# Performance work log

Measured on AMD Instinct MI355X. Metric: run time of the kernel, lower is better.

The kernel has to match this reference:

```python
import jax, jax.numpy as jnp
import numpy as np

M, B, S, D, H = 3, 32, 256, 768, 1024
LN_EPS = 1e-5


def _ln(x, g, b):
    m = jnp.mean(x, axis=-1, keepdims=True)
    v = jnp.mean((x - m) ** 2, axis=-1, keepdims=True)
    return (x - m) / jnp.sqrt(v + LN_EPS) * g + b


def setup_inputs() -> dict:
    key = jax.random.key(0)
    ks = jax.random.split(key, 16)
    sc = 0.02  # weight init scale
    return {
        "feats": jax.random.normal(ks[0], (M, B, S, D), jnp.float32),
        "Wq": jax.random.normal(ks[1], (M, D, D), jnp.float32) * sc,
        "bq": jnp.zeros((M, D), jnp.float32),
        "Wk": jax.random.normal(ks[2], (M, D, D), jnp.float32) * sc,
        "bk": jnp.zeros((M, D), jnp.float32),
        "Wv": jax.random.normal(ks[3], (M, D, D), jnp.float32) * sc,
        "bv": jnp.zeros((M, D), jnp.float32),
        "pgq_w": jax.random.normal(ks[4], (M, D), jnp.float32) * sc,
        "pgq_b": jnp.zeros((M,), jnp.float32),
        "pgk_w": jax.random.normal(ks[5], (M, D), jnp.float32) * sc,
        "pgk_b": jnp.zeros((M,), jnp.float32),
        "mu_w": jax.random.normal(ks[6], (M, D), jnp.float32) * sc,
        "mu_b": jnp.zeros((M,), jnp.float32),
        "lv_w": jax.random.normal(ks[7], (M, D), jnp.float32) * sc,
        "lv_b": jnp.zeros((M,), jnp.float32),
        "dyn": jnp.ones((1,), jnp.float32),
        "WE_w": jax.random.normal(ks[8], (M, D, D), jnp.float32) * sc,
        "WE_b": jnp.zeros((M, D), jnp.float32),
        "Wh_w": jax.random.normal(ks[9], (M, D, D), jnp.float32) * sc,
        "Wh_b": jnp.zeros((M, D), jnp.float32),
        "Wqc_w": jax.random.normal(ks[10], (M, D, D), jnp.float32) * sc,
        "Wqc_b": jnp.zeros((M, D), jnp.float32),
        "lnE_g": jnp.ones((M, D), jnp.float32),
        "lnE_b": jnp.zeros((M, D), jnp.float32),
        "lnG_g": jnp.ones((M, D), jnp.float32),
        "lnG_b": jnp.zeros((M, D), jnp.float32),
        "out_w": jax.random.normal(ks[11], (D * M, H), jnp.float32) * sc,
        "out_b": jnp.zeros((H,), jnp.float32),
        "eps": jax.random.normal(ks[12], (M, M - 1, B, S, 1), jnp.float32),
    }


def reference(feats, Wq, bq, Wk, bk, Wv, bv, pgq_w, pgq_b, pgk_w, pgk_b,
              mu_w, mu_b, lv_w, lv_b, dyn, WE_w, WE_b, Wh_w, Wh_b, Wqc_w, Wqc_b,
              lnE_g, lnE_b, lnG_g, lnG_b, out_w, out_b, eps):
    # batched per-modality projections: [M,B,S,D]
    Qs = jnp.einsum('mbsd,mde->mbse', feats, Wq) + bq[:, None, None, :]
    Ks = jnp.einsum('mbsd,mde->mbse', feats, Wk) + bk[:, None, None, :]
    Vs = jnp.einsum('mbsd,mde->mbse', feats, Wv) + bv[:, None, None, :]
    scale = 1.0 / jnp.sqrt(jnp.float32(D))

    kl = jnp.float32(0.0)
    outs = []
    for i in range(M):
        Qi = Qs[i]  # [B,S,D]
        mu = jnp.einsum('bsd,d->bs', Qi, mu_w[i])[..., None] + mu_b[i]      # [B,S,1]
        lv = jnp.einsum('bsd,d->bs', Qi, lv_w[i])[..., None] + lv_b[i]      # [B,S,1]
        std = jnp.exp(0.5 * lv)
        pq_base = jax.nn.sigmoid(
            jnp.einsum('bsd,d->bs', Qi, pgq_w[i])[..., None] + pgq_b[i])    # [B,S,1]
        kl_i = -0.5 * jnp.sum(1.0 + lv - mu ** 2 - jnp.exp(lv))
        agg = jnp.zeros_like(Qi)
        cnt = 0
        for j in range(M):
            if j == i:
                continue
            d_gate = mu + dyn * std * eps[i, cnt]  # reparameterization
            cnt += 1
            kl = kl + kl_i
            g = jax.nn.sigmoid(d_gate)             # [B,S,1]
            p_q = pq_base * g
            p_k = jax.nn.sigmoid(
                jnp.einsum('bsd,d->bs', Ks[j], pgk_w[i])[..., None] + pgk_b[i]) * g
            A = jnp.einsum('bqd,bkd->bqk', Qi, Ks[j]) * scale
            A = A * p_q * jnp.swapaxes(p_k, 1, 2)  # pregated scores
            W = jax.nn.softmax(A, axis=-1)
            agg = agg + jnp.einsum('bqk,bkd->bqd', W, Vs[j])
        # CAG
        E = jax.nn.relu(agg @ WE_w[i] + WE_b[i])
        G = jax.nn.relu(agg @ Wh_w[i] + Wh_b[i] + Qi @ Wqc_w[i] + Wqc_b[i])
        Ci = _ln(E, lnE_g[i], lnE_b[i]) * _ln(G, lnG_g[i], lnG_b[i])
        outs.append(Ci)
    fused = jnp.concatenate(outs, axis=-1)[:, 0, :]  # [B, M*D]
    out = fused @ out_w + out_b                       # [B, H]
    return out, kl
```

## Files before the change

### kernel.cpp

```cpp
#include <hip/hip_runtime.h>

#define M 3
#define B 32
#define S 256
#define D 768
#define H 1024
#define MD (M * D)
#define NP (M * (M - 1))
#define SCALE 0.03608439182435161f
#define LN_EPS 1e-5f

#define OFF_WMU   0
#define OFF_WLV   2304
#define OFF_WPGQ  4608
#define OFF_WPK   6912
#define OFF_CMU   11520
#define OFF_CLV   11523
#define OFF_CPGQ  11526
#define OFF_CPK   11529
#define OFF_PQ    11536
#define OFF_Q     11776
#define OFF_QBK   85504
#define OFF_QK    85760
#define OFF_MLH   233216
#define OFF_KLP   236288
#define OFF_FUSED 457728
#define OFF_FSUM  531520
#define OFF_WKT   1711168
#define OFF_ARENA 3480640
#define OFF_ARENA2 7019584
#define OFF_AGG   236544

__device__ __forceinline__ float wave_reduce(float v) {
    #pragma unroll
    for (int o = 32; o > 0; o >>= 1) v += __shfl_down(v, o, 64);
    return v;
}

__device__ __forceinline__ float sigmoidf(float x) {
    return 1.0f / (1.0f + __expf(-x));
}

__device__ __forceinline__ float dot4(float4 a, float4 b) {
    return a.x * b.x + a.y * b.y + a.z * b.z + a.w * b.w;
}

__device__ __forceinline__ void fma4(float4& a, float s, float4 w) {
    a.x += s * w.x; a.y += s * w.y; a.z += s * w.z; a.w += s * w.w;
}

__global__ __launch_bounds__(256) void k_prep2(const float* feats,
        const float* Wq, const float* Wk,
        const float* bq, const float* bk,
        const float* mu_w, const float* mu_b, const float* lv_w, const float* lv_b,
        const float* pgq_w, const float* pgq_b, const float* pgk_w, const float* pgk_b,
        float* ws) {
    int blk = blockIdx.x;
    if (blk < 72) {
        int mat = blk / 12, rg = blk % 12;
        const float* Wm; const float *va, *vb, *vc;
        float *oa, *ob, *oc; int nv;
        if (mat < 3) {
            int i = mat;
            Wm = Wq + i * D * D;
            va = mu_w + i * D; vb = lv_w + i * D; vc = pgq_w + i * D;
            oa = ws + OFF_WMU + i * D; ob = ws + OFF_WLV + i * D; oc = ws + OFF_WPGQ + i * D;
            nv = 3;
        } else {
            int j = mat - 3;
            int i1 = (j == 0) ? 1 : 0, i2 = (j == 2) ? 1 : 2;
            int p1 = 2 * i1 + ((j < i1) ? j : j - 1);
            int p2 = 2 * i2 + ((j < i2) ? j : j - 1);
            Wm = Wk + j * D * D;
            va = pgk_w + i1 * D; vb = pgk_w + i2 * D; vc = va;
            oa = ws + OFF_WPK + p1 * D; ob = ws + OFF_WPK + p2 * D; oc = oa;
            nv = 2;
        }
        int wave = threadIdx.x >> 6, lane = threadIdx.x & 63;
        const float4* va4 = (const float4*)va;
        const float4* vb4 = (const float4*)vb;
        const float4* vc4 = (const float4*)vc;
        float4 A0 = va4[lane], A1 = va4[lane + 64], A2 = va4[lane + 128];
        float4 B0 = vb4[lane], B1 = vb4[lane + 64], B2 = vb4[lane + 128];
        float4 C0 = vc4[lane], C1 = vc4[lane + 64], C2 = vc4[lane + 128];
        int base = rg * 64 + wave * 16;
        for (int r = 0; r < 16; r += 2) {
            const float4* rowP = (const float4*)(Wm + (base + r) * D);
            const float4* rowQ = (const float4*)(Wm + (base + r + 1) * D);
            float4 x0 = rowP[lane], x1 = rowP[lane + 64], x2 = rowP[lane + 128];
            float4 y0 = rowQ[lane], y1 = rowQ[lane + 64], y2 = rowQ[lane + 128];
            float daP = dot4(x0, A0) + dot4(x1, A1) + dot4(x2, A2);
            float dbP = dot4(x0, B0) + dot4(x1, B1) + dot4(x2, B2);
            float dcP = dot4(x0, C0) + dot4(x1, C1) + dot4(x2, C2);
            float daQ = dot4(y0, A0) + dot4(y1, A1) + dot4(y2, A2);
            float dbQ = dot4(y0, B0) + dot4(y1, B1) + dot4(y2, B2);
            float dcQ = dot4(y0, C0) + dot4(y1, C1) + dot4(y2, C2);
            daP = wave_reduce(daP); dbP = wave_reduce(dbP);
            daQ = wave_reduce(daQ); dbQ = wave_reduce(dbQ);
            if (nv == 3) { dcP = wave_reduce(dcP); dcQ = wave_reduce(dcQ); }
            if (lane == 0) {
                oa[base + r] = daP; ob[base + r] = dbP;
                oa[base + r + 1] = daQ; ob[base + r + 1] = dbQ;
                if (nv == 3) { oc[base + r] = dcP; oc[base + r + 1] = dcQ; }
            }
        }
    } else if (blk < 87) {
        int job = blk - 72;
        const float *a, *bvec; float bias; float* out;
        if (job < 3)      { int i = job;     a = bq + i * D; bvec = mu_w + i * D;  bias = mu_b[i];  out = ws + OFF_CMU + i; }
        else if (job < 6) { int i = job - 3; a = bq + i * D; bvec = lv_w + i * D;  bias = lv_b[i];  out = ws + OFF_CLV + i; }
        else if (job < 9) { int i = job - 6; a = bq + i * D; bvec = pgq_w + i * D; bias = pgq_b[i]; out = ws + OFF_CPGQ + i; }
        else {
            int p = job - 9, i = p / 2, c = p % 2, j = c + (c >= i ? 1 : 0);
            a = bk + j * D; bvec = pgk_w + i * D; bias = pgk_b[i]; out = ws + OFF_CPK + p;
        }
        int t = threadIdx.x;
        float part = 0.f;
        if (t < 192) part = dot4(((const float4*)a)[t], ((const float4*)bvec)[t]);
        part = wave_reduce(part);
        __shared__ float r[4];
        if ((t & 63) == 0) r[t >> 6] = part;
        __syncthreads();
        if (t == 0) *out = r[0] + r[1] + r[2] + r[3] + bias;
    } else if (blk < 519) {
        int r = blk - 87;
        int j = r / 144; r = r % 144;
        int d0 = (r / 12) * 64, e0 = (r % 12) * 64;
        __shared__ float tile[64][65];
        const float* src = Wk + j * D * D;
        for (int idx = threadIdx.x; idx < 4096; idx += 256) {
            int rr = idx / 64, cc = idx % 64;
            tile[rr][cc] = src[(d0 + rr) * D + e0 + cc];
        }
        __syncthreads();
        float* dst = ws + OFF_WKT + j * D * D;
        for (int idx = threadIdx.x; idx < 4096; idx += 256) {
            int rr = idx / 64, cc = idx % 64;
            dst[(e0 + rr) * D + d0 + cc] = tile[cc][rr];
        }
    } else {
        int qb = blk - 519;
        int i = qb / 96, r = qb % 96, bg = r / 24, kc = r % 24;
        int kbase = kc * 32;
        __shared__ __align__(16) float xs[32][8];
        for (int idx = threadIdx.x; idx < 256; idx += 256) {
            int d = idx & 31, bb = idx >> 5;
            xs[d][bb] = feats[((size_t)(i * B + bg * 8 + bb) * S) * D + kbase + d];
        }
        __syncthreads();
        if (threadIdx.x < 192) {
            int e4 = threadIdx.x * 4;
            const float* Wm = Wq + i * D * D + kbase * D + e4;
            float4 acc[8];
            #pragma unroll
            for (int bb = 0; bb < 8; bb++) acc[bb] = make_float4(0.f, 0.f, 0.f, 0.f);
            for (int k = 0; k < 32; k++) {
                float4 w = *(const float4*)(Wm + k * D);
                float4 x0 = *(const float4*)&xs[k][0];
                float4 x1 = *(const float4*)&xs[k][4];
                fma4(acc[0], x0.x, w); fma4(acc[1], x0.y, w);
                fma4(acc[2], x0.z, w); fma4(acc[3], x0.w, w);
                fma4(acc[4], x1.x, w); fma4(acc[5], x1.y, w);
                fma4(acc[6], x1.z, w); fma4(acc[7], x1.w, w);
            }
            #pragma unroll
            for (int bb = 0; bb < 8; bb++)
                *(float4*)&ws[OFF_ARENA + kc * 73728 + (i * 32 + bg * 8 + bb) * 768 + e4] = acc[bb];
        }
    }
}

__global__ __launch_bounds__(256) void k_redQ(const float* feats, const float* bq,
        const float* bk, const float* eps, const float* dyn, float* ws) {
    int blk = blockIdx.x;
    int i = blk / B, b = blk % B;
    int fbase = (i * B + b) * D;
    int t = threadIdx.x;
    int wave = t >> 6, lane = t & 63;
    __shared__ float4 qsh[192];
    __shared__ float redsh[8];
    __shared__ float pqred[12];
    if (t < 192) {
        float4 a = *(const float4*)&bq[i * D + t * 4];
        #pragma unroll
        for (int kc = 0; kc < 24; kc++) {
            float4 v = *(const float4*)&ws[OFF_ARENA + kc * 73728 + fbase + t * 4];
            a.x += v.x; a.y += v.y; a.z += v.z; a.w += v.w;
        }
        *(float4*)&ws[OFF_Q + fbase + t * 4] = a;
        qsh[t] = a;
    }
    __syncthreads();
    int jA = (i == 0) ? 1 : 0, jB = (i == 2) ? 1 : 2;
    float pA_ = 0.f, pB_ = 0.f;
    if (t < 192) {
        float4 q = qsh[t];
        pA_ = dot4(q, *(const float4*)&bk[jA * D + t * 4]);
        pB_ = dot4(q, *(const float4*)&bk[jB * D + t * 4]);
    }
    pA_ = wave_reduce(pA_); pB_ = wave_reduce(pB_);
    if (lane == 0) { redsh[wave] = pA_; redsh[4 + wave] = pB_; }
    float dm = 0.f, dl = 0.f, dp = 0.f;
    if (t < 192) {
        float4 x = *(const float4*)&feats[((size_t)(i * B + b) * S) * D + t * 4];
        dm = dot4(x, *(const float4*)&ws[OFF_WMU + i * D + t * 4]);
        dl = dot4(x, *(const float4*)&ws[OFF_WLV + i * D + t * 4]);
        dp = dot4(x, *(const float4*)&ws[OFF_WPGQ + i * D + t * 4]);
    }
    dm = wave_reduce(dm); dl = wave_reduce(dl); dp = wave_reduce(dp);
    if (lane == 0 && wave < 3) { pqred[wave] = dm; pqred[4 + wave] = dl; pqred[8 + wave] = dp; }
    __syncthreads();
    if (t == 0) {
        ws[OFF_QBK + (2 * i) * B + b]     = redsh[0] + redsh[1] + redsh[2] + redsh[3];
        ws[OFF_QBK + (2 * i + 1) * B + b] = redsh[4] + redsh[5] + redsh[6] + redsh[7];
        float mu0 = pqred[0] + pqred[1] + pqred[2] + ws[OFF_CMU + i];
        float lv0 = pqred[4] + pqred[5] + pqred[6] + ws[OFF_CLV + i];
        float pqb = pqred[8] + pqred[9] + pqred[10] + ws[OFF_CPGQ + i];
        float sd = dyn[0] * __expf(0.5f * lv0);
        float pqs = sigmoidf(pqb);
        #pragma unroll
        for (int c = 0; c < 2; c++) {
            int p = 2 * i + c;
            float e0 = eps[(size_t)(p * B + b) * S];
            ws[OFF_PQ + p * B + b] = pqs * sigmoidf(mu0 + sd * e0);
        }
    }
}

__global__ __launch_bounds__(256, 4) void k_qk(float* ws) {
    int blk = blockIdx.x;
    int j = blk / 192, r = blk % 192, vg = r / 24, kc = r % 24;
    int kbase = kc * 32;
    int i1 = (j == 0) ? 1 : 0, i2 = (j == 2) ? 1 : 2;
    __shared__ __align__(16) float xs[32][8];
    for (int idx = threadIdx.x; idx < 256; idx += 256) {
        int d = idx & 31, v = idx >> 5;
        int v64 = vg * 8 + v;
        int i_ = (v64 < 32) ? i1 : i2, b = v64 & 31;
        xs[d][v] = ws[OFF_Q + (i_ * 32 + b) * 768 + kbase + d];
    }
    __syncthreads();
    if (threadIdx.x < 192) {
        int e4 = threadIdx.x * 4;
        const float* Wm = ws + OFF_WKT + j * D * D + kbase * D + e4;
        float4 acc[8];
        #pragma unroll
        for (int bb = 0; bb < 8; bb++) acc[bb] = make_float4(0.f, 0.f, 0.f, 0.f);
        for (int k = 0; k < 32; k++) {
            float4 w = *(const float4*)(Wm + k * D);
            float4 x0 = *(const float4*)&xs[k][0];
            float4 x1 = *(const float4*)&xs[k][4];
            fma4(acc[0], x0.x, w); fma4(acc[1], x0.y, w);
            fma4(acc[2], x0.z, w); fma4(acc[3], x0.w, w);
            fma4(acc[4], x1.x, w); fma4(acc[5], x1.y, w);
            fma4(acc[6], x1.z, w); fma4(acc[7], x1.w, w);
        }
        #pragma unroll
        for (int v = 0; v < 8; v++)
            *(float4*)&ws[OFF_ARENA2 + kc * 147456 + (j * 64 + vg * 8 + v) * 768 + e4] = acc[v];
    }
}

__global__ __launch_bounds__(256) void k_redqk(float* ws) {
    int idx = blockIdx.x * 256 + threadIdx.x;
    int fidx = idx * 4;
    int row = fidx / 768, d = fidx % 768;
    int j = row / 64, v64 = row % 64;
    int b = v64 & 31, islot = v64 >> 5;
    int i_ = islot ? ((j == 2) ? 1 : 2) : ((j == 0) ? 1 : 0);
    int p = 2 * i_ + ((j < i_) ? j : j - 1);
    float4 a = make_float4(0.f, 0.f, 0.f, 0.f);
    #pragma unroll
    for (int kc = 0; kc < 24; kc++) {
        float4 v = *(const float4*)&ws[OFF_ARENA2 + kc * 147456 + fidx];
        a.x += v.x; a.y += v.y; a.z += v.z; a.w += v.w;
    }
    *(float4*)&ws[OFF_QK + (p * B + b) * D + d] = a;
}

__global__ __launch_bounds__(1024) void k_fused(const float* feats, const float* eps,
                                                const float* dyn, float* ws) {
    int blk = blockIdx.x;
    int b = blk >> 3, h = blk & 7;
    int t = threadIdx.x;
    int w = t >> 6, lane = t & 63;
    __shared__ __align__(16) float swA[4608];
    __shared__ __align__(16) float swPK[4608];
    __shared__ __align__(16) float sqk[4608];
    __shared__ float raws[6][32], pkps[6][32], mus[3][32], lvs[3][32], wgt[6][32];
    __shared__ float klv[96];
    __shared__ float pq_s[6], qbk_s[6], cmu_s[3], clv_s[3], cpk_s[6];
    {
        const float4* srcA = (const float4*)(ws + OFF_WMU);
        const float4* srcP = (const float4*)(ws + OFF_WPK);
        float4* dA = (float4*)swA;
        float4* dP = (float4*)swPK;
        float4* dQ = (float4*)sqk;
        for (int idx = t; idx < 1152; idx += 1024) {
            dA[idx] = srcA[idx];
            dP[idx] = srcP[idx];
            int p = idx / 192, d4 = (idx % 192) * 4;
            dQ[idx] = *(const float4*)&ws[OFF_QK + (p * B + b) * D + d4];
        }
        if (t < 6) { pq_s[t] = ws[OFF_PQ + t * B + b]; qbk_s[t] = ws[OFF_QBK + t * B + b]; cpk_s[t] = ws[OFF_CPK + t]; }
        else if (t < 9) { cmu_s[t - 6] = ws[OFF_CMU + t - 6]; clv_s[t - 6] = ws[OFF_CLV + t - 6]; }
    }
    __syncthreads();
    const float4* swA4 = (const float4*)swA;
    const float4* swPK4 = (const float4*)swPK;
    const float4* sqk4 = (const float4*)sqk;
    for (int tau = w * 6; tau < w * 6 + 6; tau++) {
        int m = tau >> 5, k = tau & 31;
        const float4* row = (const float4*)(feats + ((size_t)((m * B + b) * S) + h * 32 + k) * D);
        float4 x0 = row[lane], x1 = row[lane + 64], x2 = row[lane + 128];
        int i1 = (m == 0) ? 1 : 0, i2 = (m == 2) ? 1 : 2;
        int pj0 = 2 * i1 + ((m < i1) ? m : m - 1);
        int pj1 = 2 * i2 + ((m < i2) ? m : m - 1);
        int oM = m * 192, oL = (3 + m) * 192, o0 = pj0 * 192, o1 = pj1 * 192;
        float dmu = dot4(x0, swA4[oM + lane]) + dot4(x1, swA4[oM + lane + 64]) + dot4(x2, swA4[oM + lane + 128]);
        float dlv = dot4(x0, swA4[oL + lane]) + dot4(x1, swA4[oL + lane + 64]) + dot4(x2, swA4[oL + lane + 128]);
        float dk0 = dot4(x0, swPK4[o0 + lane]) + dot4(x1, swPK4[o0 + lane + 64]) + dot4(x2, swPK4[o0 + lane + 128]);
        float dk1 = dot4(x0, swPK4[o1 + lane]) + dot4(x1, swPK4[o1 + lane + 64]) + dot4(x2, swPK4[o1 + lane + 128]);
        float dr0 = dot4(x0, sqk4[o0 + lane]) + dot4(x1, sqk4[o0 + lane + 64]) + dot4(x2, sqk4[o0 + lane + 128]);
        float dr1 = dot4(x0, sqk4[o1 + lane]) + dot4(x1, sqk4[o1 + lane + 64]) + dot4(x2, sqk4[o1 + lane + 128]);
        dmu = wave_reduce(dmu); dlv = wave_reduce(dlv);
        dk0 = wave_reduce(dk0); dk1 = wave_reduce(dk1);
        dr0 = wave_reduce(dr0); dr1 = wave_reduce(dr1);
        if (lane == 0) {
            mus[m][k] = dmu + cmu_s[m];
            lvs[m][k] = dlv + clv_s[m];
            pkps[pj0][k] = dk0 + cpk_s[pj0];
            pkps[pj1][k] = dk1 + cpk_s[pj1];
            raws[pj0][k] = dr0;
            raws[pj1][k] = dr1;
        }
    }
    __syncthreads();
    float dynv = dyn[0];
    if (t < 192) {
        int p = t >> 5, k = t & 31;
        int iq = p >> 1;
        float e = eps[(size_t)(p * B + b) * S + h * 32 + k];
        float g = sigmoidf(mus[iq][k] + dynv * __expf(0.5f * lvs[iq][k]) * e);
        float pk = sigmoidf(pkps[p][k]) * g;
        float s = (raws[p][k] + qbk_s[p]) * SCALE * pq_s[p] * pk;
        float mc = s;
        #pragma unroll
        for (int o = 16; o > 0; o >>= 1) mc = fmaxf(mc, __shfl_xor(mc, o, 64));
        float wv_ = __expf(s - mc);
        float l = wv_;
        #pragma unroll
        for (int o = 16; o > 0; o >>= 1) l += __shfl_xor(l, o, 64);
        wgt[p][k] = wv_;
        if (k == 0) {
            float* mh = ws + OFF_MLH + (p * B + b) * 16 + h * 2;
            mh[0] = mc; mh[1] = l;
        }
    } else if (t < 288) {
        int tau = t - 192;
        int m = tau >> 5, k = tau & 31;
        float muv = mus[m][k], lvv = lvs[m][k];
        klv[tau] = 1.0f + lvv - muv * muv - __expf(lvv);
    }
    __syncthreads();
    if (t < 768) {
        #pragma unroll
        for (int jm = 0; jm < 3; jm++) {
            int i1 = (jm == 0) ? 1 : 0, i2 = (jm == 2) ? 1 : 2;
            int pj0 = 2 * i1 + ((jm < i1) ? jm : jm - 1);
            int pj1 = 2 * i2 + ((jm < i2) ? jm : jm - 1);
            const float* col = feats + ((size_t)((jm * B + b) * S) + h * 32) * D + t;
            float accA = 0.f, accB = 0.f;
            #pragma unroll 8
            for (int k = 0; k < 32; k++) {
                float fv = col[(size_t)k * D];
                accA += wgt[pj0][k] * fv;
                accB += wgt[pj1][k] * fv;
            }
            ws[OFF_FSUM + h * 147456 + (pj0 * B + b) * D + t] = accA;
            ws[OFF_FSUM + h * 147456 + (pj1 * B + b) * D + t] = accB;
        }
    }
    if (t < 64) {
        float s2 = klv[t] + ((t < 32) ? klv[64 + t] : 0.f);
        s2 = wave_reduce(s2);
        if (t == 0) ws[OFF_KLP + blk] = s2;
    }
}

__global__ __launch_bounds__(192, 4) void k_agg2(const float* Wv, float* ws) {
    int blk = blockIdx.x;
    int i = blk / 192, r = blk % 192, js = r / 96, r2 = r % 96, bg = r2 / 24, kc = r2 % 24;
    int kbase = kc * 32;
    int j0 = (i == 0) ? 1 : 0, j1 = (i == 2) ? 1 : 2;
    int jv = js ? j1 : j0;
    int p = 2 * i + js;
    __shared__ __align__(16) float xs[32][8];
    __shared__ float comb[8][8];
    if (threadIdx.x < 8) {
        int bb = threadIdx.x;
        const float* mh = ws + OFF_MLH + (p * B + bg * 8 + bb) * 16;
        float mm[8], ll[8];
        float mx = -1e30f;
        #pragma unroll
        for (int hh = 0; hh < 8; hh++) { mm[hh] = mh[2 * hh]; ll[hh] = mh[2 * hh + 1]; mx = fmaxf(mx, mm[hh]); }
        float L = 0.f;
        float ee[8];
        #pragma unroll
        for (int hh = 0; hh < 8; hh++) { ee[hh] = __expf(mm[hh] - mx); L += ee[hh] * ll[hh]; }
        #pragma unroll
        for (int hh = 0; hh < 8; hh++) comb[hh][bb] = ee[hh] / L;
    }
    __syncthreads();
    for (int idx = threadIdx.x; idx < 256; idx += 192) {
        int d = idx & 31, bb = idx >> 5;
        int base = OFF_FSUM + (p * B + bg * 8 + bb) * D + kbase + d;
        float v = 0.f;
        #pragma unroll
        for (int hh = 0; hh < 8; hh++) v += comb[hh][bb] * ws[base + hh * 147456];
        xs[d][bb] = v;
    }
    __syncthreads();
    int e4 = threadIdx.x * 4;
    const float* W0 = Wv + jv * D * D + kbase * D + e4;
    float4 acc[8];
    #pragma unroll
    for (int bb = 0; bb < 8; bb++) acc[bb] = make_float4(0.f, 0.f, 0.f, 0.f);
    for (int k = 0; k < 32; k++) {
        float4 w0 = *(const float4*)(W0 + k * D);
        float4 a0 = *(const float4*)&xs[k][0];
        float4 a1 = *(const float4*)&xs[k][4];
        fma4(acc[0], a0.x, w0); fma4(acc[1], a0.y, w0);
        fma4(acc[2], a0.z, w0); fma4(acc[3], a0.w, w0);
        fma4(acc[4], a1.x, w0); fma4(acc[5], a1.y, w0);
        fma4(acc[6], a1.z, w0); fma4(acc[7], a1.w, w0);
    }
    #pragma unroll
    for (int bb = 0; bb < 8; bb++)
        *(float4*)&ws[OFF_ARENA + (js * 24 + kc) * 73728 + (i * 32 + bg * 8 + bb) * 768 + e4] = acc[bb];
}

__global__ __launch_bounds__(256) void k_redA(const float* bv, float* ws) {
    int idx = blockIdx.x * 256 + threadIdx.x;
    int fidx = idx * 4;
    int i = fidx / 24576, e = fidx % 768;
    int j0 = (i == 0) ? 1 : 0, j1 = (i == 2) ? 1 : 2;
    float4 b0 = *(const float4*)&bv[j0 * 768 + e];
    float4 b1 = *(const float4*)&bv[j1 * 768 + e];
    float4 a = make_float4(b0.x + b1.x, b0.y + b1.y, b0.z + b1.z, b0.w + b1.w);
    #pragma unroll
    for (int s = 0; s < 48; s++) {
        float4 p = *(const float4*)&ws[OFF_ARENA + s * 73728 + fidx];
        a.x += p.x; a.y += p.y; a.z += p.z; a.w += p.w;
    }
    *(float4*)&ws[OFF_AGG + fidx] = a;
}

__global__ __launch_bounds__(192, 4) void k_eg2(const float* WE_w, const float* Wh_w,
                                                const float* Wqc_w, float* ws) {
    int blk = blockIdx.x;
    int kind = blk / 288, r = blk % 288;
    int i = r / 96, r2 = r % 96, bg = r2 / 24, kc = r2 % 24;
    int kbase = kc * 32;
    int src = (kind == 2) ? OFF_Q : OFF_AGG;
    __shared__ __align__(16) float xs[32][8];
    for (int idx = threadIdx.x; idx < 256; idx += 192) {
        int d = idx & 31, bb = idx >> 5;
        xs[d][bb] = ws[src + (i * 32 + bg * 8 + bb) * 768 + kbase + d];
    }
    __syncthreads();
    int e4 = threadIdx.x * 4;
    const float* Wm = ((kind == 0) ? WE_w : (kind == 1) ? Wh_w : Wqc_w) + i * D * D + kbase * D + e4;
    float4 acc[8];
    #pragma unroll
    for (int bb = 0; bb < 8; bb++) acc[bb] = make_float4(0.f, 0.f, 0.f, 0.f);
    for (int k = 0; k < 32; k++) {
        float4 w = *(const float4*)(Wm + k * D);
        float4 a0 = *(const float4*)&xs[k][0];
        float4 a1 = *(const float4*)&xs[k][4];
        fma4(acc[0], a0.x, w); fma4(acc[1], a0.y, w);
        fma4(acc[2], a0.z, w); fma4(acc[3], a0.w, w);
        fma4(acc[4], a1.x, w); fma4(acc[5], a1.y, w);
        fma4(acc[6], a1.z, w); fma4(acc[7], a1.w, w);
    }
    #pragma unroll
    for (int bb = 0; bb < 8; bb++)
        *(float4*)&ws[OFF_ARENA2 + (kind * 24 + kc) * 73728 + (i * 32 + bg * 8 + bb) * 768 + e4] = acc[bb];
}

__global__ __launch_bounds__(256) void k_redEGLN(const float* WE_b, const float* Wh_b,
        const float* Wqc_b,
        const float* lnE_g, const float* lnE_b,
        const float* lnG_g, const float* lnG_b, float* ws) {
    int blk = blockIdx.x;
    int i = blk / B, b = blk % B;
    int row = (i * B + b) * D;
    int t = threadIdx.x;
    float4 e = make_float4(0.f, 0.f, 0.f, 0.f);
    float4 g = make_float4(0.f, 0.f, 0.f, 0.f);
    if (t < 192) {
        e = *(const float4*)&WE_b[i * D + t * 4];
        float4 b0 = *(const float4*)&Wh_b[i * D + t * 4];
        float4 b1 = *(const float4*)&Wqc_b[i * D + t * 4];
        g = make_float4(b0.x + b1.x, b0.y + b1.y, b0.z + b1.z, b0.w + b1.w);
        #pragma unroll
        for (int s = 0; s < 24; s++) {
            float4 p = *(const float4*)&ws[OFF_ARENA2 + s * 73728 + row + t * 4];
            e.x += p.x; e.y += p.y; e.z += p.z; e.w += p.w;
        }
        #pragma unroll
        for (int s = 24; s < 72; s++) {
            float4 p = *(const float4*)&ws[OFF_ARENA2 + s * 73728 + row + t * 4];
            g.x += p.x; g.y += p.y; g.z += p.z; g.w += p.w;
        }
        e.x = fmaxf(e.x, 0.f); e.y = fmaxf(e.y, 0.f); e.z = fmaxf(e.z, 0.f); e.w = fmaxf(e.w, 0.f);
        g.x = fmaxf(g.x, 0.f); g.y = fmaxf(g.y, 0.f); g.z = fmaxf(g.z, 0.f); g.w = fmaxf(g.w, 0.f);
    }
    __shared__ float r1[256], r2[256], r3[256], r4[256];
    r1[t] = e.x + e.y + e.z + e.w;
    r2[t] = e.x * e.x + e.y * e.y + e.z * e.z + e.w * e.w;
    r3[t] = g.x + g.y + g.z + g.w;
    r4[t] = g.x * g.x + g.y * g.y + g.z * g.z + g.w * g.w;
    __syncthreads();
    for (int st = 128; st > 0; st >>= 1) {
        if (t < st) { r1[t] += r1[t + st]; r2[t] += r2[t + st]; r3[t] += r3[t + st]; r4[t] += r4[t + st]; }
        __syncthreads();
    }
    float mE = r1[0] * (1.0f / D), vE = r2[0] * (1.0f / D) - mE * mE;
    float mG = r3[0] * (1.0f / D), vG = r4[0] * (1.0f / D) - mG * mG;
    float sE = rsqrtf(vE + LN_EPS), sG = rsqrtf(vG + LN_EPS);
    if (t < 192) {
        float4 eg  = *(const float4*)&lnE_g[i * D + t * 4];
        float4 ebv = *(const float4*)&lnE_b[i * D + t * 4];
        float4 gg  = *(const float4*)&lnG_g[i * D + t * 4];
        float4 gbv = *(const float4*)&lnG_b[i * D + t * 4];
        float4 o;
        o.x = ((e.x - mE) * sE * eg.x + ebv.x) * ((g.x - mG) * sG * gg.x + gbv.x);
        o.y = ((e.y - mE) * sE * eg.y + ebv.y) * ((g.y - mG) * sG * gg.y + gbv.y);
        o.z = ((e.z - mE) * sE * eg.z + ebv.z) * ((g.z - mG) * sG * gg.z + gbv.z);
        o.w = ((e.w - mE) * sE * eg.w + ebv.w) * ((g.w - mG) * sG * gg.w + gbv.w);
        *(float4*)&ws[OFF_FUSED + b * MD + i * D + t * 4] = o;
    }
}

__global__ __launch_bounds__(256, 4) void k_out2(const float* out_w, float* ws) {
    int blk = blockIdx.x;
    int bg = blk / 72, kc = blk % 72;
    int kbase = kc * 32;
    __shared__ __align__(16) float xs[32][8];
    for (int idx = threadIdx.x; idx < 256; idx += 256) {
        int d = idx & 31, bb = idx >> 5;
        xs[d][bb] = ws[OFF_FUSED + (bg * 8 + bb) * MD + kbase + d];
    }
    __syncthreads();
    int e4 = threadIdx.x * 4;
    const float* Wm = out_w + kbase * H + e4;
    float4 acc[8];
    #pragma unroll
    for (int bb = 0; bb < 8; bb++) acc[bb] = make_float4(0.f, 0.f, 0.f, 0.f);
    for (int k = 0; k < 32; k++) {
        float4 w = *(const float4*)(Wm + k * H);
        float4 x0 = *(const float4*)&xs[k][0];
        float4 x1 = *(const float4*)&xs[k][4];
        fma4(acc[0], x0.x, w); fma4(acc[1], x0.y, w);
        fma4(acc[2], x0.z, w); fma4(acc[3], x0.w, w);
        fma4(acc[4], x1.x, w); fma4(acc[5], x1.y, w);
        fma4(acc[6], x1.z, w); fma4(acc[7], x1.w, w);
    }
    #pragma unroll
    for (int bb = 0; bb < 8; bb++)
        *(float4*)&ws[OFF_ARENA + kc * 32768 + (bg * 8 + bb) * 1024 + e4] = acc[bb];
}

__global__ __launch_bounds__(256) void k_fin(const float* out_b, float* ws, float* out) {
    int b = blockIdx.x;
    int h4 = threadIdx.x * 4;
    float4 a = *(const float4*)&out_b[h4];
    #pragma unroll
    for (int kc = 0; kc < 72; kc++) {
        float4 p = *(const float4*)&ws[OFF_ARENA + kc * 32768 + b * 1024 + h4];
        a.x += p.x; a.y += p.y; a.z += p.z; a.w += p.w;
    }
    *(float4*)&out[b * H + h4] = a;
    if (b == 0) {
        int t = threadIdx.x;
        __shared__ float kls[256];
        kls[t] = ws[OFF_KLP + t];
        __syncthreads();
        for (int st = 128; st > 0; st >>= 1) {
            if (t < st) kls[t] += kls[t + st];
            __syncthreads();
        }
        if (t == 0) out[B * H] = -kls[0];
    }
}

extern "C" void kernel_launch(void* const* d_in, const int* in_sizes, int n_in,
                              void* d_out, int out_size, void* d_ws, size_t ws_size,
                              hipStream_t stream) {
    const float* feats = (const float*)d_in[0];
    const float* Wq    = (const float*)d_in[1];
    const float* bq    = (const float*)d_in[2];
    const float* Wk    = (const float*)d_in[3];
    const float* bk    = (const float*)d_in[4];
    const float* Wv    = (const float*)d_in[5];
    const float* bv    = (const float*)d_in[6];
    const float* pgq_w = (const float*)d_in[7];
    const float* pgq_b = (const float*)d_in[8];
    const float* pgk_w = (const float*)d_in[9];
    const float* pgk_b = (const float*)d_in[10];
    const float* mu_w  = (const float*)d_in[11];
    const float* mu_b  = (const float*)d_in[12];
    const float* lv_w  = (const float*)d_in[13];
    const float* lv_b  = (const float*)d_in[14];
    const float* dyn   = (const float*)d_in[15];
    const float* WE_w  = (const float*)d_in[16];
    const float* WE_b  = (const float*)d_in[17];
    const float* Wh_w  = (const float*)d_in[18];
    const float* Wh_b  = (const float*)d_in[19];
    const float* Wqc_w = (const float*)d_in[20];
    const float* Wqc_b = (const float*)d_in[21];
    const float* lnE_g = (const float*)d_in[22];
    const float* lnE_b = (const float*)d_in[23];
    const float* lnG_g = (const float*)d_in[24];
    const float* lnG_b = (const float*)d_in[25];
    const float* out_w = (const float*)d_in[26];
    const float* out_b = (const float*)d_in[27];
    const float* eps   = (const float*)d_in[28];
    float* ws  = (float*)d_ws;
    float* out = (float*)d_out;

    k_prep2<<<807, 256, 0, stream>>>(feats, Wq, Wk, bq, bk, mu_w, mu_b, lv_w, lv_b,
                                     pgq_w, pgq_b, pgk_w, pgk_b, ws);
    k_redQ<<<96, 256, 0, stream>>>(feats, bq, bk, eps, dyn, ws);
    k_qk<<<576, 256, 0, stream>>>(ws);
    k_redqk<<<144, 256, 0, stream>>>(ws);
    k_fused<<<256, 1024, 0, stream>>>(feats, eps, dyn, ws);
    k_agg2<<<576, 192, 0, stream>>>(Wv, ws);
    k_redA<<<72, 256, 0, stream>>>(bv, ws);
    k_eg2<<<864, 192, 0, stream>>>(WE_w, Wh_w, Wqc_w, ws);
    k_redEGLN<<<96, 256, 0, stream>>>(WE_b, Wh_b, Wqc_b, lnE_g, lnE_b, lnG_g, lnG_b, ws);
    k_out2<<<288, 256, 0, stream>>>(out_w, ws);
    k_fin<<<32, 256, 0, stream>>>(out_b, ws, out);
}
```

Before: 289.3 us.

## Widen GEMV tiles to 16 rows and hoist Qi@Wqc into the QK kernel

```diff
diff --git a/kernel.cpp b/kernel.cpp
--- a/kernel.cpp
+++ b/kernel.cpp
@@ -24,12 +24,12 @@
 #define OFF_QK    85760
 #define OFF_MLH   233216
 #define OFF_KLP   236288
+#define OFF_AGG   236544
 #define OFF_FUSED 457728
 #define OFF_FSUM  531520
 #define OFF_WKT   1711168
 #define OFF_ARENA 3480640
 #define OFF_ARENA2 7019584
-#define OFF_AGG   236544
 
 __device__ __forceinline__ float wave_reduce(float v) {
     #pragma unroll
@@ -48,6 +48,33 @@
 __device__ __forceinline__ void fma4(float4& a, float s, float4 w) {
     a.x += s * w.x; a.y += s * w.y; a.z += s * w.z; a.w += s * w.w;
 }
+
+#define GEMV16_BODY(WPTR, OUTBASE, ROWBASE_EXPR)                                   \
+    {                                                                              \
+        int e4 = threadIdx.x * 4;                                                  \
+        const float* Wm = (WPTR);                                                  \
+        float4 acc[16];                                                            \
+        _Pragma("unroll")                                                          \
+        for (int v = 0; v < 16; v++) acc[v] = make_float4(0.f, 0.f, 0.f, 0.f);     \
+        for (int k = 0; k < 32; k++) {                                             \
+            float4 w = *(const float4*)(Wm + k * D);                               \
+            float4 x0 = *(const float4*)&xs[k][0];                                 \
+            float4 x1 = *(const float4*)&xs[k][4];                                 \
+            float4 x2 = *(const float4*)&xs[k][8];                                 \
+            float4 x3 = *(const float4*)&xs[k][12];                                \
+            fma4(acc[0], x0.x, w);  fma4(acc[1], x0.y, w);                         \
+            fma4(acc[2], x0.z, w);  fma4(acc[3], x0.w, w);                         \
+            fma4(acc[4], x1.x, w);  fma4(acc[5], x1.y, w);                         \
+            fma4(acc[6], x1.z, w);  fma4(acc[7], x1.w, w);                         \
+            fma4(acc[8], x2.x, w);  fma4(acc[9], x2.y, w);                         \
+            fma4(acc[10], x2.z, w); fma4(acc[11], x2.w, w);                        \
+            fma4(acc[12], x3.x, w); fma4(acc[13], x3.y, w);                        \
+            fma4(acc[14], x3.z, w); fma4(acc[15], x3.w, w);                        \
+        }                                                                          \
+        _Pragma("unroll")                                                          \
+        for (int v = 0; v < 16; v++)                                               \
+            *(float4*)&ws[(OUTBASE) + (ROWBASE_EXPR + v) * 768 + e4] = acc[v];     \
+    }
 
 __global__ __launch_bounds__(256) void k_prep2(const float* feats,
         const float* Wq, const float* Wk,
@@ -140,32 +167,17 @@
         }
     } else {
         int qb = blk - 519;
-        int i = qb / 96, r = qb % 96, bg = r / 24, kc = r % 24;
+        int i = qb / 48, r = qb % 48, bg = r / 24, kc = r % 24;
         int kbase = kc * 32;
-        __shared__ __align__(16) float xs[32][8];
-        for (int idx = threadIdx.x; idx < 256; idx += 256) {
+        __shared__ __align__(16) float xs[32][16];
+        for (int idx = threadIdx.x; idx < 512; idx += 256) {
             int d = idx & 31, bb = idx >> 5;
-            xs[d][bb] = feats[((size_t)(i * B + bg * 8 + bb) * S) * D + kbase + d];
+            xs[d][bb] = feats[((size_t)(i * B + bg * 16 + bb) * S) * D + kbase + d];
         }
         __syncthreads();
         if (threadIdx.x < 192) {
-            int e4 = threadIdx.x * 4;
-            const float* Wm = Wq + i * D * D + kbase * D + e4;
-            float4 acc[8];
-            #pragma unroll
-            for (int bb = 0; bb < 8; bb++) acc[bb] = make_float4(0.f, 0.f, 0.f, 0.f);
-            for (int k = 0; k < 32; k++) {
-                float4 w = *(const float4*)(Wm + k * D);
-                float4 x0 = *(const float4*)&xs[k][0];
-                float4 x1 = *(const float4*)&xs[k][4];
-                fma4(acc[0], x0.x, w); fma4(acc[1], x0.y, w);
-                fma4(acc[2], x0.z, w); fma4(acc[3], x0.w, w);
-                fma4(acc[4], x1.x, w); fma4(acc[5], x1.y, w);
-                fma4(acc[6], x1.z, w); fma4(acc[7], x1.w, w);
-            }
-            #pragma unroll
-            for (int bb = 0; bb < 8; bb++)
-                *(float4*)&ws[OFF_ARENA + kc * 73728 + (i * 32 + bg * 8 + bb) * 768 + e4] = acc[bb];
+            GEMV16_BODY(Wq + i * D * D + kbase * D + threadIdx.x * 4,
+                        OFF_ARENA + kc * 73728, (i * 32 + bg * 16))
         }
     }
 }
@@ -227,48 +239,49 @@
     }
 }
 
-__global__ __launch_bounds__(256, 4) void k_qk(float* ws) {
-    int blk = blockIdx.x;
-    int j = blk / 192, r = blk % 192, vg = r / 24, kc = r % 24;
-    int kbase = kc * 32;
-    int i1 = (j == 0) ? 1 : 0, i2 = (j == 2) ? 1 : 2;
-    __shared__ __align__(16) float xs[32][8];
-    for (int idx = threadIdx.x; idx < 256; idx += 256) {
-        int d = idx & 31, v = idx >> 5;
-        int v64 = vg * 8 + v;
-        int i_ = (v64 < 32) ? i1 : i2, b = v64 & 31;
-        xs[d][v] = ws[OFF_Q + (i_ * 32 + b) * 768 + kbase + d];
-    }
-    __syncthreads();
-    if (threadIdx.x < 192) {
-        int e4 = threadIdx.x * 4;
-        const float* Wm = ws + OFF_WKT + j * D * D + kbase * D + e4;
-        float4 acc[8];
-        #pragma unroll
-        for (int bb = 0; bb < 8; bb++) acc[bb] = make_float4(0.f, 0.f, 0.f, 0.f);
-        for (int k = 0; k < 32; k++) {
-            float4 w = *(const float4*)(Wm + k * D);
-            float4 x0 = *(const float4*)&xs[k][0];
-            float4 x1 = *(const float4*)&xs[k][4];
-            fma4(acc[0], x0.x, w); fma4(acc[1], x0.y, w);
-            fma4(acc[2], x0.z, w); fma4(acc[3], x0.w, w);
-            fma4(acc[4], x1.x, w); fma4(acc[5], x1.y, w);
-            fma4(acc[6], x1.z, w); fma4(acc[7], x1.w, w);
-        }
-        #pragma unroll
-        for (int v = 0; v < 8; v++)
-            *(float4*)&ws[OFF_ARENA2 + kc * 147456 + (j * 64 + vg * 8 + v) * 768 + e4] = acc[v];
+__global__ __launch_bounds__(192, 4) void k_qk(const float* Wqc_w, float* ws) {
+    int blk = blockIdx.x;
+    __shared__ __align__(16) float xs[32][16];
+    if (blk < 288) {
+        int j = blk / 96, r = blk % 96, vg = r / 24, kc = r % 24;
+        int kbase = kc * 32;
+        int i1 = (j == 0) ? 1 : 0, i2 = (j == 2) ? 1 : 2;
+        for (int idx = threadIdx.x; idx < 512; idx += 192) {
+            int d = idx & 31, v = idx >> 5;
+            int v16 = vg * 16 + v;
+            int i_ = (v16 < 32) ? i1 : i2, b = v16 & 31;
+            xs[d][v] = ws[OFF_Q + (i_ * 32 + b) * 768 + kbase + d];
+        }
+        __syncthreads();
+        if (threadIdx.x < 192) {
+            GEMV16_BODY(ws + OFF_WKT + j * D * D + kbase * D + threadIdx.x * 4,
+                        OFF_ARENA2 + kc * 147456, (j * 64 + vg * 16))
+        }
+    } else {
+        int q2 = blk - 288;
+        int i = q2 / 48, r2 = q2 % 48, bg = r2 / 24, kc = r2 % 24;
+        int kbase = kc * 32;
+        for (int idx = threadIdx.x; idx < 512; idx += 192) {
+            int d = idx & 31, v = idx >> 5;
+            xs[d][v] = ws[OFF_Q + (i * B + bg * 16 + v) * 768 + kbase + d];
+        }
+        __syncthreads();
+        if (threadIdx.x < 192) {
+            GEMV16_BODY(Wqc_w + i * D * D + kbase * D + threadIdx.x * 4,
+                        OFF_ARENA2 + (48 + kc) * 73728, (i * 32 + bg * 16))
+        }
     }
 }
 
 __global__ __launch_bounds__(256) void k_redqk(float* ws) {
     int idx = blockIdx.x * 256 + threadIdx.x;
     int fidx = idx * 4;
-    int row = fidx / 768, d = fidx % 768;
+    int row = fidx / 768;
     int j = row / 64, v64 = row % 64;
     int b = v64 & 31, islot = v64 >> 5;
     int i_ = islot ? ((j == 2) ? 1 : 2) : ((j == 0) ? 1 : 0);
     int p = 2 * i_ + ((j < i_) ? j : j - 1);
+    int d = fidx % 768;
     float4 a = make_float4(0.f, 0.f, 0.f, 0.f);
     #pragma unroll
     for (int kc = 0; kc < 24; kc++) {
@@ -388,18 +401,18 @@
     }
 }
 
-__global__ __launch_bounds__(192, 4) void k_agg2(const float* Wv, float* ws) {
-    int blk = blockIdx.x;
-    int i = blk / 192, r = blk % 192, js = r / 96, r2 = r % 96, bg = r2 / 24, kc = r2 % 24;
+__global__ __launch_bounds__(192, 3) void k_agg2(const float* Wv, float* ws) {
+    int blk = blockIdx.x;
+    int i = blk / 96, r = blk % 96, js = r / 48, r2 = r % 48, bg = r2 / 24, kc = r2 % 24;
     int kbase = kc * 32;
     int j0 = (i == 0) ? 1 : 0, j1 = (i == 2) ? 1 : 2;
     int jv = js ? j1 : j0;
     int p = 2 * i + js;
-    __shared__ __align__(16) float xs[32][8];
-    __shared__ float comb[8][8];
-    if (threadIdx.x < 8) {
+    __shared__ __align__(16) float xs[32][16];
+    __shared__ float comb[8][16];
+    if (threadIdx.x < 16) {
         int bb = threadIdx.x;
-        const float* mh = ws + OFF_MLH + (p * B + bg * 8 + bb) * 16;
+        const float* mh = ws + OFF_MLH + (p * B + bg * 16 + bb) * 16;
         float mm[8], ll[8];
         float mx = -1e30f;
         #pragma unroll
@@ -412,32 +425,19 @@
         for (int hh = 0; hh < 8; hh++) comb[hh][bb] = ee[hh] / L;
     }
     __syncthreads();
-    for (int idx = threadIdx.x; idx < 256; idx += 192) {
+    for (int idx = threadIdx.x; idx < 512; idx += 192) {
         int d = idx & 31, bb = idx >> 5;
-        int base = OFF_FSUM + (p * B + bg * 8 + bb) * D + kbase + d;
+        int base = OFF_FSUM + (p * B + bg * 16 + bb) * D + kbase + d;
         float v = 0.f;
         #pragma unroll
         for (int hh = 0; hh < 8; hh++) v += comb[hh][bb] * ws[base + hh * 147456];
         xs[d][bb] = v;
     }
     __syncthreads();
-    int e4 = threadIdx.x * 4;
-    const float* W0 = Wv + jv * D * D + kbase * D + e4;
-    float4 acc[8];
-    #pragma unroll
-    for (int bb = 0; bb < 8; bb++) acc[bb] = make_float4(0.f, 0.f, 0.f, 0.f);
-    for (int k = 0; k < 32; k++) {
-        float4 w0 = *(const float4*)(W0 + k * D);
-        float4 a0 = *(const float4*)&xs[k][0];
-        float4 a1 = *(const float4*)&xs[k][4];
-        fma4(acc[0], a0.x, w0); fma4(acc[1], a0.y, w0);
-        fma4(acc[2], a0.z, w0); fma4(acc[3], a0.w, w0);
-        fma4(acc[4], a1.x, w0); fma4(acc[5], a1.y, w0);
-        fma4(acc[6], a1.z, w0); fma4(acc[7], a1.w, w0);
-    }
-    #pragma unroll
-    for (int bb = 0; bb < 8; bb++)
-        *(float4*)&ws[OFF_ARENA + (js * 24 + kc) * 73728 + (i * 32 + bg * 8 + bb) * 768 + e4] = acc[bb];
+    if (threadIdx.x < 192) {
+        GEMV16_BODY(Wv + jv * D * D + kbase * D + threadIdx.x * 4,
+                    OFF_ARENA + (js * 24 + kc) * 73728, (i * 32 + bg * 16))
+    }
 }
 
 __global__ __launch_bounds__(256) void k_redA(const float* bv, float* ws) {
@@ -457,35 +457,21 @@
 }
 
 __global__ __launch_bounds__(192, 4) void k_eg2(const float* WE_w, const float* Wh_w,
-                                                const float* Wqc_w, float* ws) {
-    int blk = blockIdx.x;
-    int kind = blk / 288, r = blk % 288;
-    int i = r / 96, r2 = r % 96, bg = r2 / 24, kc = r2 % 24;
+                                                float* ws) {
+    int blk = blockIdx.x;
+    int kind = blk / 144, r = blk % 144;
+    int i = r / 48, r2 = r % 48, bg = r2 / 24, kc = r2 % 24;
     int kbase = kc * 32;
-    int src = (kind == 2) ? OFF_Q : OFF_AGG;
-    __shared__ __align__(16) float xs[32][8];
-    for (int idx = threadIdx.x; idx < 256; idx += 192) {
+    __shared__ __align__(16) float xs[32][16];
+    for (int idx = threadIdx.x; idx < 512; idx += 192) {
         int d = idx & 31, bb = idx >> 5;
-        xs[d][bb] = ws[src + (i * 32 + bg * 8 + bb) * 768 + kbase + d];
-    }
-    __syncthreads();
-    int e4 = threadIdx.x * 4;
-    const float* Wm = ((kind == 0) ? WE_w : (kind == 1) ? Wh_w : Wqc_w) + i * D * D + kbase * D + e4;
-    float4 acc[8];
-    #pragma unroll
-    for (int bb = 0; bb < 8; bb++) acc[bb] = make_float4(0.f, 0.f, 0.f, 0.f);
-    for (int k = 0; k < 32; k++) {
-        float4 w = *(const float4*)(Wm + k * D);
-        float4 a0 = *(const float4*)&xs[k][0];
-        float4 a1 = *(const float4*)&xs[k][4];
-        fma4(acc[0], a0.x, w); fma4(acc[1], a0.y, w);
-        fma4(acc[2], a0.z, w); fma4(acc[3], a0.w, w);
-        fma4(acc[4], a1.x, w); fma4(acc[5], a1.y, w);
-        fma4(acc[6], a1.z, w); fma4(acc[7], a1.w, w);
-    }
-    #pragma unroll
-    for (int bb = 0; bb < 8; bb++)
-        *(float4*)&ws[OFF_ARENA2 + (kind * 24 + kc) * 73728 + (i * 32 + bg * 8 + bb) * 768 + e4] = acc[bb];
+        xs[d][bb] = ws[OFF_AGG + (i * 32 + bg * 16 + bb) * 768 + kbase + d];
+    }
+    __syncthreads();
+    if (threadIdx.x < 192) {
+        GEMV16_BODY(((kind == 0) ? WE_w : Wh_w) + i * D * D + kbase * D + threadIdx.x * 4,
+                    OFF_ARENA2 + (kind * 24 + kc) * 73728, (i * 32 + bg * 16))
+    }
 }
 
 __global__ __launch_bounds__(256) void k_redEGLN(const float* WE_b, const float* Wh_b,
@@ -547,29 +533,35 @@
     int blk = blockIdx.x;
     int bg = blk / 72, kc = blk % 72;
     int kbase = kc * 32;
-    __shared__ __align__(16) float xs[32][8];
-    for (int idx = threadIdx.x; idx < 256; idx += 256) {
+    __shared__ __align__(16) float xs[32][16];
+    for (int idx = threadIdx.x; idx < 512; idx += 256) {
         int d = idx & 31, bb = idx >> 5;
-        xs[d][bb] = ws[OFF_FUSED + (bg * 8 + bb) * MD + kbase + d];
+        xs[d][bb] = ws[OFF_FUSED + (bg * 16 + bb) * MD + kbase + d];
     }
     __syncthreads();
     int e4 = threadIdx.x * 4;
     const float* Wm = out_w + kbase * H + e4;
-    float4 acc[8];
+    float4 acc[16];
     #pragma unroll
-    for (int bb = 0; bb < 8; bb++) acc[bb] = make_float4(0.f, 0.f, 0.f, 0.f);
+    for (int v = 0; v < 16; v++) acc[v] = make_float4(0.f, 0.f, 0.f, 0.f);
     for (int k = 0; k < 32; k++) {
         float4 w = *(const float4*)(Wm + k * H);
         float4 x0 = *(const float4*)&xs[k][0];
         float4 x1 = *(const float4*)&xs[k][4];
-        fma4(acc[0], x0.x, w); fma4(acc[1], x0.y, w);
-        fma4(acc[2], x0.z, w); fma4(acc[3], x0.w, w);
-        fma4(acc[4], x1.x, w); fma4(acc[5], x1.y, w);
-        fma4(acc[6], x1.z, w); fma4(acc[7], x1.w, w);
+        float4 x2 = *(const float4*)&xs[k][8];
+        float4 x3 = *(const float4*)&xs[k][12];
+        fma4(acc[0], x0.x, w);  fma4(acc[1], x0.y, w);
+        fma4(acc[2], x0.z, w);  fma4(acc[3], x0.w, w);
+        fma4(acc[4], x1.x, w);  fma4(acc[5], x1.y, w);
+        fma4(acc[6], x1.z, w);  fma4(acc[7], x1.w, w);
+        fma4(acc[8], x2.x, w);  fma4(acc[9], x2.y, w);
+        fma4(acc[10], x2.z, w); fma4(acc[11], x2.w, w);
+        fma4(acc[12], x3.x, w); fma4(acc[13], x3.y, w);
+        fma4(acc[14], x3.z, w); fma4(acc[15], x3.w, w);
     }
     #pragma unroll
-    for (int bb = 0; bb < 8; bb++)
-        *(float4*)&ws[OFF_ARENA + kc * 32768 + (bg * 8 + bb) * 1024 + e4] = acc[bb];
+    for (int v = 0; v < 16; v++)
+        *(float4*)&ws[OFF_ARENA + kc * 32768 + (bg * 16 + v) * 1024 + e4] = acc[v];
 }
 
 __global__ __launch_bounds__(256) void k_fin(const float* out_b, float* ws, float* out) {
@@ -630,16 +622,16 @@
     float* ws  = (float*)d_ws;
     float* out = (float*)d_out;
 
-    k_prep2<<<807, 256, 0, stream>>>(feats, Wq, Wk, bq, bk, mu_w, mu_b, lv_w, lv_b,
+    k_prep2<<<663, 256, 0, stream>>>(feats, Wq, Wk, bq, bk, mu_w, mu_b, lv_w, lv_b,
                                      pgq_w, pgq_b, pgk_w, pgk_b, ws);
     k_redQ<<<96, 256, 0, stream>>>(feats, bq, bk, eps, dyn, ws);
-    k_qk<<<576, 256, 0, stream>>>(ws);
+    k_qk<<<432, 192, 0, stream>>>(Wqc_w, ws);
     k_redqk<<<144, 256, 0, stream>>>(ws);
     k_fused<<<256, 1024, 0, stream>>>(feats, eps, dyn, ws);
-    k_agg2<<<576, 192, 0, stream>>>(Wv, ws);
+    k_agg2<<<288, 192, 0, stream>>>(Wv, ws);
     k_redA<<<72, 256, 0, stream>>>(bv, ws);
-    k_eg2<<<864, 192, 0, stream>>>(WE_w, Wh_w, Wqc_w, ws);
+    k_eg2<<<288, 192, 0, stream>>>(WE_w, Wh_w, ws);
     k_redEGLN<<<96, 256, 0, stream>>>(WE_b, Wh_b, Wqc_b, lnE_g, lnE_b, lnG_g, lnG_b, ws);
-    k_out2<<<288, 256, 0, stream>>>(out_w, ws);
+    k_out2<<<144, 256, 0, stream>>>(out_w, ws);
     k_fin<<<32, 256, 0, stream>>>(out_b, ws, out);
 }
```

After: 314.4 us. 1.09x slower.
